# Kernel tuning notes

Hardware: AMD Instinct MI355X
Metric: run time of the kernel (lower is better)

## Reference

```python
import jax, jax.numpy as jnp
import numpy as np

B, T, D, E, K, OUT = 512, 2048, 32, 64, 8, 1024  # batch, tokens, feat(=32 hardcoded), experts, top-k, expert out dim


def setup_inputs() -> dict:
    key = jax.random.key(0)
    k0, k1, k2, k3 = jax.random.split(key, 4)
    x = jax.random.normal(k0, (B, T, D), jnp.float32)
    gate_w = jax.random.normal(k1, (E, D), jnp.float32) / np.sqrt(D)
    gate_b = jnp.zeros((E,), jnp.float32)
    # stacked expert Linear(32*k -> OUT): weight [E, OUT, D*K], bias [E, OUT]
    expert_w = jax.random.normal(k2, (E, OUT, D * K), jnp.float32) / np.sqrt(D * K)
    expert_b = jnp.zeros((E, OUT), jnp.float32)
    # gumbel noise for multinomial-without-replacement sampling (Gumbel top-k trick)
    gumbel = jax.random.gumbel(k3, (B, E, T), jnp.float32)
    return {"x": x, "gate_w": gate_w, "gate_b": gate_b,
            "expert_w": expert_w, "expert_b": expert_b, "gumbel": gumbel}


def reference(x, gate_w, gate_b, expert_w, expert_b, gumbel):
    # gate logits [B,T,E]; softmax over TOKEN axis (dim=-2 in torch)
    logits = jnp.einsum('btd,ed->bte', x, gate_w) + gate_b
    logp = jax.nn.log_softmax(logits, axis=-2)          # [B,T,E]
    # g = probs transposed to [B,E,T]; multinomial(k, no replacement) == top-k of log p + Gumbel
    scores = jnp.transpose(logp, (0, 2, 1)) + gumbel    # [B,E,T]
    _, idx = jax.lax.top_k(scores, K)                   # [B,E,K] sampled token indices
    # gather k tokens per (batch, expert): [B,E,K,D]
    gathered = jnp.take_along_axis(x[:, None, :, :], idx[..., None], axis=2)
    inp = gathered.reshape(B, E, K * D)                 # token-major concat, matches torch reshape
    # grouped per-expert GEMM + bias -> [B,E,OUT]
    out = jnp.einsum('bef,eof->beo', inp, expert_w) + expert_b[None]
    return out
```

## Files before the change

kernel.cpp:

```cpp
#include <hip/hip_runtime.h>
#include <hip/hip_bf16.h>
#include <stdint.h>

#define Bb   512
#define Tt   2048
#define Dd   32
#define Ee   64
#define Kk   8
#define OUTn 1024

typedef __attribute__((ext_vector_type(4))) float f32x4;
typedef __attribute__((ext_vector_type(8))) short short8;
typedef __attribute__((ext_vector_type(4))) unsigned int uint4v;

static __device__ __forceinline__ uint32_t f2bf(float f) {
  uint32_t u = __float_as_uint(f);
  return (u + 0x7FFFu + ((u >> 16) & 1u)) >> 16;
}
static __device__ __forceinline__ uint32_t umax32(uint32_t a, uint32_t b){ return a > b ? a : b; }
static __device__ __forceinline__ uint32_t umin32(uint32_t a, uint32_t b){ return a < b ? a : b; }

__global__ __launch_bounds__(512, 4) void kA_select(
    const float* __restrict__ x,
    const float* __restrict__ gate_w,
    const float* __restrict__ gumbel,
    uint16_t* __restrict__ inp)
{
  const int b    = blockIdx.x;
  const int tid  = threadIdx.x;
  const int wave = tid >> 6;
  const int lane = tid & 63;
  const int l15  = lane & 15;
  const int l4   = lane >> 4;
  const int c    = wave & 3;
  const int h    = wave >> 2;

  __shared__ uint32_t cand[Ee][32];

  short8 gfrag;
  {
    const float* gp = gate_w + (size_t)(c * 16 + l15) * Dd + l4 * 8;
    f32x4 g0 = *(const f32x4*)(gp);
    f32x4 g1 = *(const f32x4*)(gp + 4);
    gfrag[0] = (short)f2bf(g0[0]); gfrag[1] = (short)f2bf(g0[1]);
    gfrag[2] = (short)f2bf(g0[2]); gfrag[3] = (short)f2bf(g0[3]);
    gfrag[4] = (short)f2bf(g1[0]); gfrag[5] = (short)f2bf(g1[1]);
    gfrag[6] = (short)f2bf(g1[2]); gfrag[7] = (short)f2bf(g1[3]);
  }

  uint32_t s[4][8];
  #pragma unroll
  for (int r = 0; r < 4; ++r)
    #pragma unroll
    for (int j = 0; j < 8; ++j) s[r][j] = 0u;

  const float* gum_base = gumbel + ((size_t)b * Ee + c * 16 + l4 * 4) * Tt + h * 1024 + l15;
  const float* x_base   = x + ((size_t)b * Tt + h * 1024 + l15) * Dd + l4 * 8;
  const int    tbase    = h * 1024 + l15;

  auto load_set = [&](float (&G)[8], f32x4 (&XV)[4], int ii) {
    #pragma unroll
    for (int ss = 0; ss < 2; ++ss) {
      #pragma unroll
      for (int r = 0; r < 4; ++r)
        G[ss * 4 + r] = gum_base[(size_t)r * Tt + ii * 32 + ss * 16];
      #pragma unroll
      for (int hv = 0; hv < 2; ++hv)
        XV[ss * 2 + hv] = *(const f32x4*)(x_base + (size_t)(ii * 32 + ss * 16) * Dd + hv * 4);
    }
  };

  auto proc_set = [&](float (&G)[8], f32x4 (&XV)[4], int ii) {
    #pragma unroll
    for (int ss = 0; ss < 2; ++ss) {
      f32x4 lo = XV[ss * 2], hi = XV[ss * 2 + 1];
      short8 bfr;
      bfr[0] = (short)f2bf(lo[0]); bfr[1] = (short)f2bf(lo[1]);
      bfr[2] = (short)f2bf(lo[2]); bfr[3] = (short)f2bf(lo[3]);
      bfr[4] = (short)f2bf(hi[0]); bfr[5] = (short)f2bf(hi[1]);
      bfr[6] = (short)f2bf(hi[2]); bfr[7] = (short)f2bf(hi[3]);
      f32x4 acc = {0.f, 0.f, 0.f, 0.f};
      acc = __builtin_amdgcn_mfma_f32_16x16x32_bf16(gfrag, bfr, acc, 0, 0, 0);
      const uint32_t tl = 2047u - (uint32_t)(tbase + ii * 32 + ss * 16);
      #pragma unroll
      for (int r = 0; r < 4; ++r) {
        float sc = acc[r] + G[ss * 4 + r];
        uint32_t u = __float_as_uint(sc);
        u = (u & 0x80000000u) ? ~u : (u | 0x80000000u);
        uint32_t key = (u & 0xFFFFF800u) | tl;
        uint32_t cc = umax32(s[r][7], key);
        uint32_t dd;
        dd = s[r][6]; s[r][7] = umin32(dd, cc); cc = umax32(dd, cc);
        dd = s[r][5]; s[r][6] = umin32(dd, cc); cc = umax32(dd, cc);
        dd = s[r][4]; s[r][5] = umin32(dd, cc); cc = umax32(dd, cc);
        dd = s[r][3]; s[r][4] = umin32(dd, cc); cc = umax32(dd, cc);
        dd = s[r][2]; s[r][3] = umin32(dd, cc); cc = umax32(dd, cc);
        dd = s[r][1]; s[r][2] = umin32(dd, cc); cc = umax32(dd, cc);
        dd = s[r][0]; s[r][1] = umin32(dd, cc); s[r][0] = umax32(dd, cc);
      }
    }
  };

  float gA[8]; f32x4 xA[4];
  float gB[8]; f32x4 xB[4];
  load_set(gA, xA, 0);
  for (int i = 0; i < 32; i += 2) {
    load_set(gB, xB, i + 1);
    proc_set(gA, xA, i);
    load_set(gA, xA, (i + 2 < 32) ? (i + 2) : 0);
    proc_set(gB, xB, i + 1);
  }

  #pragma unroll
  for (int r = 0; r < 4; ++r) {
    const int e_abs = c * 16 + l4 * 4 + r;
    #pragma unroll
    for (int rnd = 0; rnd < 16; ++rnd) {
      uint32_t cur = s[r][0];
      uint32_t mx = cur;
      mx = umax32(mx, (uint32_t)__shfl_xor((int)mx, 1));
      mx = umax32(mx, (uint32_t)__shfl_xor((int)mx, 2));
      mx = umax32(mx, (uint32_t)__shfl_xor((int)mx, 4));
      mx = umax32(mx, (uint32_t)__shfl_xor((int)mx, 8));
      if (l15 == rnd) cand[e_abs][h * 16 + rnd] = mx;
      const bool pop = (cur == mx);
      s[r][0] = pop ? s[r][1] : s[r][0];
      s[r][1] = pop ? s[r][2] : s[r][1];
      s[r][2] = pop ? s[r][3] : s[r][2];
      s[r][3] = pop ? s[r][4] : s[r][3];
      s[r][4] = pop ? s[r][5] : s[r][4];
      s[r][5] = pop ? s[r][6] : s[r][5];
      s[r][6] = pop ? s[r][7] : s[r][6];
      s[r][7] = pop ? 0u      : s[r][7];
    }
  }
  __syncthreads();

  #pragma unroll 1
  for (int el = 0; el < 8; ++el) {
    const int e = wave * 8 + el;
    const bool alive = lane < 32;
    uint32_t myT = 2047;
    double v = -1e300;
    if (alive) {
      uint32_t key = cand[e][lane];
      myT = 2047u - (key & 2047u);
      const float* xr = x + ((size_t)b * Tt + myT) * Dd;
      const float* gr = gate_w + (size_t)e * Dd;
      double a = 0.0;
      #pragma unroll
      for (int d = 0; d < Dd; ++d) a += (double)xr[d] * (double)gr[d];
      v = a + (double)gumbel[((size_t)b * Ee + e) * Tt + myT];
    }
    uint32_t ti = alive ? myT : 0xFFFFu;
    uint32_t ord[8];
    #pragma unroll
    for (int k = 0; k < 8; ++k) {
      double bv = v; uint32_t bt = ti;
      #pragma unroll
      for (int off = 1; off < 64; off <<= 1) {
        double   ov = __shfl_xor(bv, off);
        uint32_t ot = (uint32_t)__shfl_xor((int)bt, off);
        if (ov > bv || (ov == bv && ot < bt)) { bv = ov; bt = ot; }
      }
      ord[k] = bt;
      if (ti == bt) v = -1e300;
    }

    const int kk = lane >> 3, sub = lane & 7;
    uint32_t tk = ord[0];
    #pragma unroll
    for (int q = 1; q < 8; ++q) tk = (kk == q) ? ord[q] : tk;
    const float* xs = x + ((size_t)b * Tt + tk) * Dd + sub * 4;
    f32x4 xv = *(const f32x4*)xs;
    uint32_t p0 = f2bf(xv[0]) | (f2bf(xv[1]) << 16);
    uint32_t p1 = f2bf(xv[2]) | (f2bf(xv[3]) << 16);
    uint32_t* dst = (uint32_t*)inp + ((((size_t)b * Ee + e) * 256) + kk * 32 + sub * 4) / 2;
    dst[0] = p0; dst[1] = p1;
  }
}

__global__ __launch_bounds__(256) void kB_gemm(
    const uint16_t* __restrict__ inp,
    const float* __restrict__ expert_w,
    const float* __restrict__ expert_b,
    float* __restrict__ out)
{
  const int bid = blockIdx.x;
  const int xcd = bid & 7;
  const int idx = bid >> 3;
  const int e   = xcd * 8 + (idx >> 5);
  const int rem = idx & 31;
  const int mb  = rem >> 3;
  const int nb  = rem & 7;
  const int b0 = mb * 128;
  const int o0 = nb * 128;
  const int tid  = threadIdx.x;
  const int wave = tid >> 6;
  const int lane = tid & 63;
  const int l15 = lane & 15, l4 = lane >> 4;
  const int wm = (wave & 1) * 64;
  const int wn = (wave >> 1) * 64;

  __shared__ __attribute__((aligned(16))) uint32_t Al[128 * 32];
  __shared__ __attribute__((aligned(16))) uint32_t Wl[128 * 32];

  f32x4 acc[4][4];
  #pragma unroll
  for (int i = 0; i < 4; ++i)
    #pragma unroll
    for (int j = 0; j < 4; ++j) acc[i][j] = (f32x4){0.f, 0.f, 0.f, 0.f};

  for (int ks = 0; ks < 4; ++ks) {
    #pragma unroll
    for (int i = 0; i < 4; ++i) {
      int gi = tid + i * 256;
      int m = gi >> 3, q = gi & 7;
      const uint4v* src = (const uint4v*)(inp + ((size_t)(b0 + m) * Ee + e) * 256 + ks * 64 + q * 8);
      *(uint4v*)&Al[m * 32 + ((q ^ (m & 7)) * 4)] = *src;
    }
    #pragma unroll
    for (int i = 0; i < 4; ++i) {
      int gi = tid + i * 256;
      int o = gi >> 3, q = gi & 7;
      const float* src = expert_w + ((size_t)e * OUTn + o0 + o) * 256 + ks * 64 + q * 8;
      f32x4 w0 = *(const f32x4*)src;
      f32x4 w1 = *(const f32x4*)(src + 4);
      uint4v v;
      v[0] = f2bf(w0[0]) | (f2bf(w0[1]) << 16);
      v[1] = f2bf(w0[2]) | (f2bf(w0[3]) << 16);
      v[2] = f2bf(w1[0]) | (f2bf(w1[1]) << 16);
      v[3] = f2bf(w1[2]) | (f2bf(w1[3]) << 16);
      *(uint4v*)&Wl[o * 32 + ((q ^ (o & 7)) * 4)] = v;
    }
    __syncthreads();

    short8 af[4][2], bf[4][2];
    #pragma unroll
    for (int mf = 0; mf < 4; ++mf)
      #pragma unroll
      for (int kb = 0; kb < 2; ++kb) {
        int row = wm + mf * 16 + l15;
        int g = kb * 4 + l4;
        af[mf][kb] = *(const short8*)&Al[row * 32 + ((g ^ (row & 7)) * 4)];
      }
    #pragma unroll
    for (int nf = 0; nf < 4; ++nf)
      #pragma unroll
      for (int kb = 0; kb < 2; ++kb) {
        int row = wn + nf * 16 + l15;
        int g = kb * 4 + l4;
        bf[nf][kb] = *(const short8*)&Wl[row * 32 + ((g ^ (row & 7)) * 4)];
      }
    #pragma unroll
    for (int mf = 0; mf < 4; ++mf)
      #pragma unroll
      for (int nf = 0; nf < 4; ++nf)
        #pragma unroll
        for (int kb = 0; kb < 2; ++kb)
          acc[mf][nf] = __builtin_amdgcn_mfma_f32_16x16x32_bf16(af[mf][kb], bf[nf][kb], acc[mf][nf], 0, 0, 0);
    __syncthreads();
  }

  #pragma unroll
  for (int nf = 0; nf < 4; ++nf) {
    const int ocol = o0 + wn + nf * 16 + l15;
    const float bias = expert_b[(size_t)e * OUTn + ocol];
    #pragma unroll
    for (int mf = 0; mf < 4; ++mf) {
      #pragma unroll
      for (int reg = 0; reg < 4; ++reg) {
        const int mrow = b0 + wm + mf * 16 + l4 * 4 + reg;
        out[((size_t)mrow * Ee + e) * OUTn + ocol] = acc[mf][nf][reg] + bias;
      }
    }
  }
}

extern "C" void kernel_launch(void* const* d_in, const int* in_sizes, int n_in,
                              void* d_out, int out_size, void* d_ws, size_t ws_size,
                              hipStream_t stream) {
  const float* x        = (const float*)d_in[0];
  const float* gate_w   = (const float*)d_in[1];
  const float* expert_w = (const float*)d_in[3];
  const float* expert_b = (const float*)d_in[4];
  const float* gumbel   = (const float*)d_in[5];

  uint16_t* inp = (uint16_t*)d_ws;

  kA_select<<<Bb, 512, 0, stream>>>(x, gate_w, gumbel, inp);
  kB_gemm<<<2048, 256, 0, stream>>>(inp, expert_w, expert_b, (float*)d_out);
}
```

Measured before the change: 246.3 us.

## Stage x and gumbel tiles into LDS via async global_load_lds double buffering

Rewrites the selection kernel's main loop so that x and gumbel tiles are copied directly into shared memory with global_load_lds, double-buffered across 64-token stages with waitcnt and barriers. The block shrinks from 512 to 256 threads (4 waves): each wave now owns 16 experts over the whole token range instead of splitting tokens into two halves, so the candidate list per expert drops from 32 to 16. The aim is to overlap global memory latency with the MFMA and sorting-network work and to cut per-thread register loads. In exchange it adds barrier synchronisation, uses more LDS, and gives each wave twice as many tokens to process.

```diff
diff --git a/kernel.cpp b/kernel.cpp
--- a/kernel.cpp
+++ b/kernel.cpp
@@ -20,7 +20,7 @@
 static __device__ __forceinline__ uint32_t umax32(uint32_t a, uint32_t b){ return a > b ? a : b; }
 static __device__ __forceinline__ uint32_t umin32(uint32_t a, uint32_t b){ return a < b ? a : b; }
 
-__global__ __launch_bounds__(512, 4) void kA_select(
+__global__ __launch_bounds__(256, 2) void kA_select(
     const float* __restrict__ x,
     const float* __restrict__ gate_w,
     const float* __restrict__ gumbel,
@@ -32,14 +32,14 @@
   const int lane = tid & 63;
   const int l15  = lane & 15;
   const int l4   = lane >> 4;
-  const int c    = wave & 3;
-  const int h    = wave >> 2;
-
-  __shared__ uint32_t cand[Ee][32];
+
+  __shared__ __attribute__((aligned(16))) float xb[2 * 2048];
+  __shared__ __attribute__((aligned(16))) float gbuf[2 * 4096];
+  __shared__ uint32_t cand[Ee][16];
 
   short8 gfrag;
   {
-    const float* gp = gate_w + (size_t)(c * 16 + l15) * Dd + l4 * 8;
+    const float* gp = gate_w + (size_t)(wave * 16 + l15) * Dd + l4 * 8;
     f32x4 g0 = *(const f32x4*)(gp);
     f32x4 g1 = *(const f32x4*)(gp + 4);
     gfrag[0] = (short)f2bf(g0[0]); gfrag[1] = (short)f2bf(g0[1]);
@@ -54,37 +54,47 @@
     #pragma unroll
     for (int j = 0; j < 8; ++j) s[r][j] = 0u;
 
-  const float* gum_base = gumbel + ((size_t)b * Ee + c * 16 + l4 * 4) * Tt + h * 1024 + l15;
-  const float* x_base   = x + ((size_t)b * Tt + h * 1024 + l15) * Dd + l4 * 8;
-  const int    tbase    = h * 1024 + l15;
-
-  auto load_set = [&](float (&G)[8], f32x4 (&XV)[4], int ii) {
-    #pragma unroll
-    for (int ss = 0; ss < 2; ++ss) {
-      #pragma unroll
-      for (int r = 0; r < 4; ++r)
-        G[ss * 4 + r] = gum_base[(size_t)r * Tt + ii * 32 + ss * 16];
-      #pragma unroll
-      for (int hv = 0; hv < 2; ++hv)
-        XV[ss * 2 + hv] = *(const f32x4*)(x_base + (size_t)(ii * 32 + ss * 16) * Dd + hv * 4);
+  const float* xtile = x + (size_t)b * Tt * Dd;
+  const float* grow  = gumbel + ((size_t)b * Ee + wave * 16) * Tt + lane;
+
+  auto stage = [&](int st, int bf) {
+    #pragma unroll
+    for (int i = 0; i < 2; ++i) {
+      const int tok = i * 32 + wave * 8 + (lane >> 3);
+      const float* src = xtile + (size_t)(st * 64 + tok) * Dd + (((lane & 7) ^ (lane >> 3)) << 2);
+      float* dst = &xb[bf * 2048 + (i * 256 + wave * 64) * 4];
+      __builtin_amdgcn_global_load_lds(
+          (const __attribute__((address_space(1))) void*)src,
+          (__attribute__((address_space(3))) void*)dst, 16, 0, 0);
+    }
+    #pragma unroll
+    for (int e = 0; e < 16; ++e) {
+      const float* src = grow + (size_t)e * Tt + st * 64;
+      float* dst = &gbuf[bf * 4096 + wave * 1024 + e * 64];
+      __builtin_amdgcn_global_load_lds(
+          (const __attribute__((address_space(1))) void*)src,
+          (__attribute__((address_space(3))) void*)dst, 4, 0, 0);
     }
   };
 
-  auto proc_set = [&](float (&G)[8], f32x4 (&XV)[4], int ii) {
-    #pragma unroll
-    for (int ss = 0; ss < 2; ++ss) {
-      f32x4 lo = XV[ss * 2], hi = XV[ss * 2 + 1];
+  auto compute = [&](int st, int bf) {
+    #pragma unroll
+    for (int g = 0; g < 4; ++g) {
+      const int tok  = g * 16 + l15;
+      const int base = bf * 2048 + tok * 32;
+      f32x4 xv0 = *(const f32x4*)&xb[base + (((l4 * 2 + 0) ^ (tok & 7)) << 2)];
+      f32x4 xv1 = *(const f32x4*)&xb[base + (((l4 * 2 + 1) ^ (tok & 7)) << 2)];
       short8 bfr;
-      bfr[0] = (short)f2bf(lo[0]); bfr[1] = (short)f2bf(lo[1]);
-      bfr[2] = (short)f2bf(lo[2]); bfr[3] = (short)f2bf(lo[3]);
-      bfr[4] = (short)f2bf(hi[0]); bfr[5] = (short)f2bf(hi[1]);
-      bfr[6] = (short)f2bf(hi[2]); bfr[7] = (short)f2bf(hi[3]);
+      bfr[0] = (short)f2bf(xv0[0]); bfr[1] = (short)f2bf(xv0[1]);
+      bfr[2] = (short)f2bf(xv0[2]); bfr[3] = (short)f2bf(xv0[3]);
+      bfr[4] = (short)f2bf(xv1[0]); bfr[5] = (short)f2bf(xv1[1]);
+      bfr[6] = (short)f2bf(xv1[2]); bfr[7] = (short)f2bf(xv1[3]);
       f32x4 acc = {0.f, 0.f, 0.f, 0.f};
       acc = __builtin_amdgcn_mfma_f32_16x16x32_bf16(gfrag, bfr, acc, 0, 0, 0);
-      const uint32_t tl = 2047u - (uint32_t)(tbase + ii * 32 + ss * 16);
+      const uint32_t tl = 2047u - (uint32_t)(st * 64 + g * 16 + l15);
       #pragma unroll
       for (int r = 0; r < 4; ++r) {
-        float sc = acc[r] + G[ss * 4 + r];
+        float sc = acc[r] + gbuf[bf * 4096 + wave * 1024 + (l4 * 4 + r) * 64 + g * 16 + l15];
         uint32_t u = __float_as_uint(sc);
         u = (u & 0x80000000u) ? ~u : (u | 0x80000000u);
         uint32_t key = (u & 0xFFFFF800u) | tl;
@@ -101,19 +111,22 @@
     }
   };
 
-  float gA[8]; f32x4 xA[4];
-  float gB[8]; f32x4 xB[4];
-  load_set(gA, xA, 0);
-  for (int i = 0; i < 32; i += 2) {
-    load_set(gB, xB, i + 1);
-    proc_set(gA, xA, i);
-    load_set(gA, xA, (i + 2 < 32) ? (i + 2) : 0);
-    proc_set(gB, xB, i + 1);
+  stage(0, 0);
+  for (int i = 0; i < 32; ++i) {
+    if (i < 31) {
+      stage(i + 1, (i + 1) & 1);
+      asm volatile("s_waitcnt vmcnt(18)" ::: "memory");
+    } else {
+      asm volatile("s_waitcnt vmcnt(0)" ::: "memory");
+    }
+    __builtin_amdgcn_s_barrier();
+    compute(i, i & 1);
+    __builtin_amdgcn_s_barrier();
   }
 
   #pragma unroll
   for (int r = 0; r < 4; ++r) {
-    const int e_abs = c * 16 + l4 * 4 + r;
+    const int e_abs = wave * 16 + l4 * 4 + r;
     #pragma unroll
     for (int rnd = 0; rnd < 16; ++rnd) {
       uint32_t cur = s[r][0];
@@ -122,7 +135,7 @@
       mx = umax32(mx, (uint32_t)__shfl_xor((int)mx, 2));
       mx = umax32(mx, (uint32_t)__shfl_xor((int)mx, 4));
       mx = umax32(mx, (uint32_t)__shfl_xor((int)mx, 8));
-      if (l15 == rnd) cand[e_abs][h * 16 + rnd] = mx;
+      if (l15 == rnd) cand[e_abs][rnd] = mx;
       const bool pop = (cur == mx);
       s[r][0] = pop ? s[r][1] : s[r][0];
       s[r][1] = pop ? s[r][2] : s[r][1];
@@ -137,9 +150,9 @@
   __syncthreads();
 
   #pragma unroll 1
-  for (int el = 0; el < 8; ++el) {
-    const int e = wave * 8 + el;
-    const bool alive = lane < 32;
+  for (int el = 0; el < 16; ++el) {
+    const int e = wave * 16 + el;
+    const bool alive = lane < 16;
     uint32_t myT = 2047;
     double v = -1e300;
     if (alive) {
@@ -288,6 +301,6 @@
 
   uint16_t* inp = (uint16_t*)d_ws;
 
-  kA_select<<<Bb, 512, 0, stream>>>(x, gate_w, gumbel, inp);
+  kA_select<<<Bb, 256, 0, stream>>>(x, gate_w, gumbel, inp);
   kB_gemm<<<2048, 256, 0, stream>>>(inp, expert_w, expert_b, (float*)d_out);
 }
```

Result: slower. 276.0 us (+12.0%).

## Stage gumbel via async global-to-LDS loads with 1024-thread select blocks

Applied to the files above, without the earlier changes.

The select kernel now uses 1024 threads per batch, splitting the token range into four quarters instead of two, so each wave handles 512 tokens and contributes 8 candidates per expert. Gumbel noise is double-buffered into shared memory with global_load_lds and explicit vmcnt waits, replacing the register double-buffering of per-lane scalar loads. The aim is better memory-level parallelism and coalescing on the gumbel stream, the largest input. In exchange, the 64 KB of shared memory and the larger block size limit occupancy, and the hand-counted waitcnt values must match the number of loads in flight.

```diff
diff --git a/kernel.cpp b/kernel.cpp
--- a/kernel.cpp
+++ b/kernel.cpp
@@ -20,7 +20,7 @@
 static __device__ __forceinline__ uint32_t umax32(uint32_t a, uint32_t b){ return a > b ? a : b; }
 static __device__ __forceinline__ uint32_t umin32(uint32_t a, uint32_t b){ return a < b ? a : b; }
 
-__global__ __launch_bounds__(512, 4) void kA_select(
+__global__ __launch_bounds__(1024) void kA_select(
     const float* __restrict__ x,
     const float* __restrict__ gate_w,
     const float* __restrict__ gumbel,
@@ -33,8 +33,9 @@
   const int l15  = lane & 15;
   const int l4   = lane >> 4;
   const int c    = wave & 3;
-  const int h    = wave >> 2;
-
+  const int q    = wave >> 2;
+
+  __shared__ __attribute__((aligned(16))) float gbuf[16 * 1024];
   __shared__ uint32_t cand[Ee][32];
 
   short8 gfrag;
@@ -54,26 +55,27 @@
     #pragma unroll
     for (int j = 0; j < 8; ++j) s[r][j] = 0u;
 
-  const float* gum_base = gumbel + ((size_t)b * Ee + c * 16 + l4 * 4) * Tt + h * 1024 + l15;
-  const float* x_base   = x + ((size_t)b * Tt + h * 1024 + l15) * Dd + l4 * 8;
-  const int    tbase    = h * 1024 + l15;
-
-  auto load_set = [&](float (&G)[8], f32x4 (&XV)[4], int ii) {
-    #pragma unroll
-    for (int ss = 0; ss < 2; ++ss) {
-      #pragma unroll
-      for (int r = 0; r < 4; ++r)
-        G[ss * 4 + r] = gum_base[(size_t)r * Tt + ii * 32 + ss * 16];
-      #pragma unroll
-      for (int hv = 0; hv < 2; ++hv)
-        XV[ss * 2 + hv] = *(const f32x4*)(x_base + (size_t)(ii * 32 + ss * 16) * Dd + hv * 4);
+  const float* gchunk = gumbel + ((size_t)b * Ee + c * 16) * Tt + q * 512;
+  const int v0 = (lane >> 5) * Tt + (lane & 31);
+  const int v1 = (lane >> 5) * Tt + ((lane & 31) ^ 16);
+  const float* xq = x + ((size_t)b * Tt + q * 512 + l15) * Dd + l4 * 8;
+
+  auto stage = [&](int st, int bf) {
+    #pragma unroll
+    for (int j = 0; j < 8; ++j) {
+      const float* src = gchunk + j * 2 * Tt + st * 32 + (((j >> 1) & 1) ? v1 : v0);
+      float* dst = &gbuf[wave * 1024 + bf * 512 + j * 64];
+      __builtin_amdgcn_global_load_lds(
+          (const __attribute__((address_space(1))) void*)src,
+          (__attribute__((address_space(3))) void*)dst, 4, 0, 0);
     }
   };
 
-  auto proc_set = [&](float (&G)[8], f32x4 (&XV)[4], int ii) {
-    #pragma unroll
-    for (int ss = 0; ss < 2; ++ss) {
-      f32x4 lo = XV[ss * 2], hi = XV[ss * 2 + 1];
+  auto compute = [&](int st, int bf, f32x4 (&xv)[4]) {
+    const int sbase = wave * 1024 + bf * 512;
+    #pragma unroll
+    for (int g = 0; g < 2; ++g) {
+      f32x4 lo = xv[g * 2], hi = xv[g * 2 + 1];
       short8 bfr;
       bfr[0] = (short)f2bf(lo[0]); bfr[1] = (short)f2bf(lo[1]);
       bfr[2] = (short)f2bf(lo[2]); bfr[3] = (short)f2bf(lo[3]);
@@ -81,10 +83,11 @@
       bfr[6] = (short)f2bf(hi[2]); bfr[7] = (short)f2bf(hi[3]);
       f32x4 acc = {0.f, 0.f, 0.f, 0.f};
       acc = __builtin_amdgcn_mfma_f32_16x16x32_bf16(gfrag, bfr, acc, 0, 0, 0);
-      const uint32_t tl = 2047u - (uint32_t)(tbase + ii * 32 + ss * 16);
+      const uint32_t tl = 2047u - (uint32_t)(q * 512 + st * 32 + g * 16 + l15);
+      const int p = (g * 16 + l15) ^ ((l4 & 1) * 16);
       #pragma unroll
       for (int r = 0; r < 4; ++r) {
-        float sc = acc[r] + G[ss * 4 + r];
+        float sc = acc[r] + gbuf[sbase + (l4 * 4 + r) * 32 + p];
         uint32_t u = __float_as_uint(sc);
         u = (u & 0x80000000u) ? ~u : (u | 0x80000000u);
         uint32_t key = (u & 0xFFFFF800u) | tl;
@@ -101,28 +104,36 @@
     }
   };
 
-  float gA[8]; f32x4 xA[4];
-  float gB[8]; f32x4 xB[4];
-  load_set(gA, xA, 0);
-  for (int i = 0; i < 32; i += 2) {
-    load_set(gB, xB, i + 1);
-    proc_set(gA, xA, i);
-    load_set(gA, xA, (i + 2 < 32) ? (i + 2) : 0);
-    proc_set(gB, xB, i + 1);
+  stage(0, 0);
+  for (int i = 0; i < 16; ++i) {
+    f32x4 xv[4];
+    #pragma unroll
+    for (int g = 0; g < 2; ++g)
+      #pragma unroll
+      for (int hv = 0; hv < 2; ++hv)
+        xv[g * 2 + hv] = *(const f32x4*)(xq + (size_t)(i * 32 + g * 16) * Dd + hv * 4);
+    if (i < 15) {
+      stage(i + 1, (i + 1) & 1);
+      asm volatile("s_waitcnt vmcnt(12)" ::: "memory");
+    } else {
+      asm volatile("s_waitcnt vmcnt(4)" ::: "memory");
+    }
+    __builtin_amdgcn_sched_barrier(0);
+    compute(i, i & 1, xv);
   }
 
   #pragma unroll
   for (int r = 0; r < 4; ++r) {
     const int e_abs = c * 16 + l4 * 4 + r;
     #pragma unroll
-    for (int rnd = 0; rnd < 16; ++rnd) {
+    for (int rnd = 0; rnd < 8; ++rnd) {
       uint32_t cur = s[r][0];
       uint32_t mx = cur;
       mx = umax32(mx, (uint32_t)__shfl_xor((int)mx, 1));
       mx = umax32(mx, (uint32_t)__shfl_xor((int)mx, 2));
       mx = umax32(mx, (uint32_t)__shfl_xor((int)mx, 4));
       mx = umax32(mx, (uint32_t)__shfl_xor((int)mx, 8));
-      if (l15 == rnd) cand[e_abs][h * 16 + rnd] = mx;
+      if (l15 == rnd) cand[e_abs][q * 8 + rnd] = mx;
       const bool pop = (cur == mx);
       s[r][0] = pop ? s[r][1] : s[r][0];
       s[r][1] = pop ? s[r][2] : s[r][1];
@@ -137,8 +148,8 @@
   __syncthreads();
 
   #pragma unroll 1
-  for (int el = 0; el < 8; ++el) {
-    const int e = wave * 8 + el;
+  for (int el = 0; el < 4; ++el) {
+    const int e = wave * 4 + el;
     const bool alive = lane < 32;
     uint32_t myT = 2047;
     double v = -1e300;
@@ -170,7 +181,7 @@
     const int kk = lane >> 3, sub = lane & 7;
     uint32_t tk = ord[0];
     #pragma unroll
-    for (int q = 1; q < 8; ++q) tk = (kk == q) ? ord[q] : tk;
+    for (int qq = 1; qq < 8; ++qq) tk = (kk == qq) ? ord[qq] : tk;
     const float* xs = x + ((size_t)b * Tt + tk) * Dd + sub * 4;
     f32x4 xv = *(const f32x4*)xs;
     uint32_t p0 = f2bf(xv[0]) | (f2bf(xv[1]) << 16);
@@ -215,15 +226,15 @@
     #pragma unroll
     for (int i = 0; i < 4; ++i) {
       int gi = tid + i * 256;
-      int m = gi >> 3, q = gi & 7;
-      const uint4v* src = (const uint4v*)(inp + ((size_t)(b0 + m) * Ee + e) * 256 + ks * 64 + q * 8);
-      *(uint4v*)&Al[m * 32 + ((q ^ (m & 7)) * 4)] = *src;
+      int m = gi >> 3, qq = gi & 7;
+      const uint4v* src = (const uint4v*)(inp + ((size_t)(b0 + m) * Ee + e) * 256 + ks * 64 + qq * 8);
+      *(uint4v*)&Al[m * 32 + ((qq ^ (m & 7)) * 4)] = *src;
     }
     #pragma unroll
     for (int i = 0; i < 4; ++i) {
       int gi = tid + i * 256;
-      int o = gi >> 3, q = gi & 7;
-      const float* src = expert_w + ((size_t)e * OUTn + o0 + o) * 256 + ks * 64 + q * 8;
+      int o = gi >> 3, qq = gi & 7;
+      const float* src = expert_w + ((size_t)e * OUTn + o0 + o) * 256 + ks * 64 + qq * 8;
       f32x4 w0 = *(const f32x4*)src;
       f32x4 w1 = *(const f32x4*)(src + 4);
       uint4v v;
@@ -231,7 +242,7 @@
       v[1] = f2bf(w0[2]) | (f2bf(w0[3]) << 16);
       v[2] = f2bf(w1[0]) | (f2bf(w1[1]) << 16);
       v[3] = f2bf(w1[2]) | (f2bf(w1[3]) << 16);
-      *(uint4v*)&Wl[o * 32 + ((q ^ (o & 7)) * 4)] = v;
+      *(uint4v*)&Wl[o * 32 + ((qq ^ (o & 7)) * 4)] = v;
     }
     __syncthreads();
 
@@ -288,6 +299,6 @@
 
   uint16_t* inp = (uint16_t*)d_ws;
 
-  kA_select<<<Bb, 512, 0, stream>>>(x, gate_w, gumbel, inp);
+  kA_select<<<Bb, 1024, 0, stream>>>(x, gate_w, gumbel, inp);
   kB_gemm<<<2048, 256, 0, stream>>>(inp, expert_w, expert_b, (float*)d_out);
 }
```

After: 247.3 us. No clear change (+0.4%).
